# Kernel optimization log

Hardware: AMD Instinct MI355X
Metric: run time of the kernel (lower is better)

Reference implementation:

```python
import jax, jax.numpy as jnp
import numpy as np

B, T, H, V, S = 64, 32, 512, 32000, 400


def setup_inputs() -> dict:
    key = jax.random.key(0)
    ks = jax.random.split(key, 14)
    f = lambda k, s: jax.random.normal(k, s, dtype=jnp.float32)
    return {
        "inputs": jax.random.randint(ks[0], (B, T), 0, V),
        "embedding0": f(ks[1], (B, H)),
        "output0": f(ks[2], (B, H)),
        "tree_h0": f(ks[3], (B, H)),
        "tree_c0": f(ks[4], (B, H)),
        "tree_context": f(ks[5], (B, S, H)),
        "text_h0": f(ks[6], (B, H)),
        "text_c0": f(ks[7], (B, H)),
        "text_context": f(ks[8], (B, S, H)),
        "word_emb": f(ks[9], (V, H)) * 0.02,
        "Wx": f(ks[10], (2 * H, 4 * H)) * 0.02,   # LSTM input weights (input_size = 2H)
        "Wh": f(ks[11], (H, 4 * H)) * 0.02,       # LSTM recurrent weights
        "b": jnp.zeros((4 * H,), jnp.float32),
        "W_in": f(ks[12], (H, H)) * 0.02,         # attention score projection
        "W_out": f(ks[13], (4 * H, H)) * 0.02,    # attention combine projection
    }


def _lstm_cell(x, h, c, Wx, Wh, b):
    g = x @ Wx + h @ Wh + b                      # [B,4H]
    i, f, gg, o = jnp.split(g, 4, axis=-1)
    c_new = jax.nn.sigmoid(f) * c + jax.nn.sigmoid(i) * jnp.tanh(gg)
    h_new = jax.nn.sigmoid(o) * jnp.tanh(c_new)
    return h_new, c_new


def _attend(h, ctx, W_in):
    target = h @ W_in                             # [B,H]
    scores = jnp.einsum('bsh,bh->bs', ctx, target)
    attn = jax.nn.softmax(scores, axis=-1)
    return jnp.einsum('bs,bsh->bh', attn, ctx)    # weighted context [B,H]


def reference(inputs, embedding0, output0, tree_h0, tree_c0, tree_context,
              text_h0, text_c0, text_context, word_emb, Wx, Wh, b, W_in, W_out):
    embeddings = word_emb[inputs]                 # [B,T,H]
    embeddings = jnp.transpose(embeddings, (1, 0, 2))  # time-major [T,B,H]

    def step(carry, emb_i):
        emb, out, th, tc, xh, xc = carry
        x = jnp.concatenate([emb, out], axis=1)   # [B,2H]
        th, tc = _lstm_cell(x, th, tc, Wx, Wh, b)  # tree branch (shared weights)
        xh, xc = _lstm_cell(x, xh, xc, Wx, Wh, b)  # text branch (shared weights)
        w_tree = _attend(th, tree_context, W_in)
        w_text = _attend(xh, text_context, W_in)
        combined = jnp.concatenate([w_tree, w_text, th, xh], axis=1)  # [B,4H]
        out = jnp.tanh(combined @ W_out)           # dropout = identity (eval mode)
        return (emb_i, out, th, tc, xh, xc), out

    carry0 = (embedding0, output0, tree_h0, tree_c0, text_h0, text_c0)
    _, outs = jax.lax.scan(step, carry0, embeddings)  # outs: [T,B,H]
    return jnp.transpose(outs, (1, 0, 2))             # [B,T,H]
```

## Files before the change

### kernel.cpp

```cpp
#include <hip/hip_runtime.h>
#include <hip/hip_bf16.h>
#include <math.h>

#define BB 64
#define TT 32
#define HH 512
#define H2 1024
#define H4 2048
#define SS 400

#define OFF_WT_HI 0u
#define OFF_WT_LO 1572864u
#define OFF_WIT_HI 3145728u
#define OFF_WIT_LO 3276800u
#define OFF_EH    3407872u
#define OFF_EL    3932160u
#define OFF_OH    4456448u
#define OFF_OL    4472832u
#define OFF_HHP   4489216u
#define OFF_HLP   4521984u
#define OFF_TC    4554752u
#define OFF_XC    4620288u
#define OFF_TH    4685824u
#define OFF_XH    4751360u
#define OFF_G     4816896u
#define OFF_TGTP  6914048u
#define OFF_PACC  7438336u
#define OFF_PML   7962624u
#define OFF_CTX16 7964672u
#define WS_NEED_F 21071872u
#define OFF_WOT_HI 21071872u
#define OFF_WOT_LO 21596160u
#define OFF_COMBH  22120448u
#define OFF_COMBL  22153216u
#define WS_NEED2_F 22185984u
#define OFF_PART  OFF_G

typedef short bf16x8 __attribute__((ext_vector_type(8)));
typedef float f32x4  __attribute__((ext_vector_type(4)));

__device__ __forceinline__ float sigm(float x){ return 1.f/(1.f+__expf(-x)); }

__device__ __forceinline__ unsigned short bf_rn(float x){
  unsigned int u = __float_as_uint(x);
  return (unsigned short)((u + 0x7fffu + ((u>>16)&1u)) >> 16);
}
__device__ __forceinline__ void split2(float x, unsigned short &h, unsigned short &l){
  h = bf_rn(x);
  float hf = __uint_as_float(((unsigned int)h)<<16);
  l = bf_rn(x - hf);
}
__device__ __forceinline__ float blo(unsigned int u){ return __uint_as_float(u<<16); }
__device__ __forceinline__ float bhi(unsigned int u){ return __uint_as_float(u & 0xffff0000u); }

__global__ __launch_bounds__(256) void k_wprep(const float* __restrict__ Wx,
    const float* __restrict__ Wh, unsigned short* __restrict__ wt_hi,
    unsigned short* __restrict__ wt_lo){
  __shared__ float lds[64][68];
  int bk = blockIdx.x >> 5, bn = blockIdx.x & 31;
  int k0 = bk*64, n0 = bn*64;
  int tid = threadIdx.x;
  #pragma unroll
  for (int i=0;i<4;i++){
    int flat = tid + i*256;
    int k = flat >> 4, nq = flat & 15;
    int kg = k0 + k;
    const float* srow = (kg < 1024) ? Wx + (size_t)kg*H4 : Wh + (size_t)(kg-1024)*H4;
    float4 v = *(const float4*)(srow + n0 + nq*4);
    *(float4*)&lds[k][nq*4] = v;
  }
  __syncthreads();
  #pragma unroll
  for (int i=0;i<2;i++){
    int flat = tid + i*256;
    int n = flat >> 3, k8 = flat & 7;
    ushort4 h0, h1, l0, l1;
    unsigned short h[8], l[8];
    #pragma unroll
    for (int j=0;j<8;j++) split2(lds[k8*8+j][n], h[j], l[j]);
    h0.x=h[0];h0.y=h[1];h0.z=h[2];h0.w=h[3]; h1.x=h[4];h1.y=h[5];h1.z=h[6];h1.w=h[7];
    l0.x=l[0];l0.y=l[1];l0.z=l[2];l0.w=l[3]; l1.x=l[4];l1.y=l[5];l1.z=l[6];l1.w=l[7];
    size_t dst = (size_t)(n0+n)*1536 + k0 + k8*8;
    *(ushort4*)(wt_hi+dst) = h0; *(ushort4*)(wt_hi+dst+4) = h1;
    *(ushort4*)(wt_lo+dst) = l0; *(ushort4*)(wt_lo+dst+4) = l1;
  }
}

__global__ __launch_bounds__(256) void k_wiprep(const float* __restrict__ W_in,
    unsigned short* __restrict__ wit_hi, unsigned short* __restrict__ wit_lo){
  __shared__ float lds[64][68];
  int bk = blockIdx.x >> 3, bn = blockIdx.x & 7;
  int k0 = bk*64, n0 = bn*64;
  int tid = threadIdx.x;
  #pragma unroll
  for (int i=0;i<4;i++){
    int flat = tid + i*256;
    int k = flat >> 4, nq = flat & 15;
    float4 v = *(const float4*)(W_in + (size_t)(k0+k)*HH + n0 + nq*4);
    *(float4*)&lds[k][nq*4] = v;
  }
  __syncthreads();
  #pragma unroll
  for (int i=0;i<2;i++){
    int flat = tid + i*256;
    int n = flat >> 3, k8 = flat & 7;
    ushort4 h0, h1, l0, l1;
    unsigned short h[8], l[8];
    #pragma unroll
    for (int j=0;j<8;j++) split2(lds[k8*8+j][n], h[j], l[j]);
    h0.x=h[0];h0.y=h[1];h0.z=h[2];h0.w=h[3]; h1.x=h[4];h1.y=h[5];h1.z=h[6];h1.w=h[7];
    l0.x=l[0];l0.y=l[1];l0.z=l[2];l0.w=l[3]; l1.x=l[4];l1.y=l[5];l1.z=l[6];l1.w=l[7];
    size_t dst = (size_t)(n0+n)*HH + k0 + k8*8;
    *(ushort4*)(wit_hi+dst) = h0; *(ushort4*)(wit_hi+dst+4) = h1;
    *(ushort4*)(wit_lo+dst) = l0; *(ushort4*)(wit_lo+dst+4) = l1;
  }
}

__global__ __launch_bounds__(256) void k_woprep(const float* __restrict__ W_out,
    unsigned short* __restrict__ wot_hi, unsigned short* __restrict__ wot_lo){
  __shared__ float lds[64][68];
  int bk = blockIdx.x >> 3, bn = blockIdx.x & 7;
  int k0 = bk*64, n0 = bn*64;
  int tid = threadIdx.x;
  #pragma unroll
  for (int i=0;i<4;i++){
    int flat = tid + i*256;
    int k = flat >> 4, nq = flat & 15;
    float4 v = *(const float4*)(W_out + (size_t)(k0+k)*HH + n0 + nq*4);
    *(float4*)&lds[k][nq*4] = v;
  }
  __syncthreads();
  #pragma unroll
  for (int i=0;i<2;i++){
    int flat = tid + i*256;
    int n = flat >> 3, k8 = flat & 7;
    ushort4 h0, h1, l0, l1;
    unsigned short h[8], l[8];
    #pragma unroll
    for (int j=0;j<8;j++) split2(lds[k8*8+j][n], h[j], l[j]);
    h0.x=h[0];h0.y=h[1];h0.z=h[2];h0.w=h[3]; h1.x=h[4];h1.y=h[5];h1.z=h[6];h1.w=h[7];
    l0.x=l[0];l0.y=l[1];l0.z=l[2];l0.w=l[3]; l1.x=l[4];l1.y=l[5];l1.z=l[6];l1.w=l[7];
    size_t dst = (size_t)(n0+n)*H4 + k0 + k8*8;
    *(ushort4*)(wot_hi+dst) = h0; *(ushort4*)(wot_hi+dst+4) = h1;
    *(ushort4*)(wot_lo+dst) = l0; *(ushort4*)(wot_lo+dst+4) = l1;
  }
}

__global__ __launch_bounds__(256) void k_ctx16(const float* __restrict__ trctx,
    const float* __restrict__ txctx, unsigned short* __restrict__ ctx16){
  size_t gid = (size_t)blockIdx.x*256 + threadIdx.x;
  size_t off = gid*8;
  const size_t CH = (size_t)BB*SS*HH;
  const float* src = (off < CH) ? trctx + off : txctx + (off - CH);
  float4 a = *(const float4*)src;
  float4 c = *(const float4*)(src+4);
  ushort4 u0, u1;
  u0.x=bf_rn(a.x); u0.y=bf_rn(a.y); u0.z=bf_rn(a.z); u0.w=bf_rn(a.w);
  u1.x=bf_rn(c.x); u1.y=bf_rn(c.y); u1.z=bf_rn(c.z); u1.w=bf_rn(c.w);
  *(ushort4*)(ctx16+off) = u0;
  *(ushort4*)(ctx16+off+4) = u1;
}

__global__ __launch_bounds__(128) void k_prep(const int* __restrict__ inp,
    const float* __restrict__ emb0, const float* __restrict__ wemb,
    unsigned short* __restrict__ eh, unsigned short* __restrict__ el){
  int n = blockIdx.x; int t = n >> 6, b = n & 63;
  const float* src = (t==0) ? emb0 + (size_t)b*HH
                            : wemb + (size_t)inp[b*TT + (t-1)]*HH;
  float4 v = ((const float4*)src)[threadIdx.x];
  ushort4 h, l;
  split2(v.x,h.x,l.x); split2(v.y,h.y,l.y); split2(v.z,h.z,l.z); split2(v.w,h.w,l.w);
  size_t base = ((size_t)t*BB + b)*HH + threadIdx.x*4;
  *(ushort4*)(eh+base) = h; *(ushort4*)(el+base) = l;
}

__global__ __launch_bounds__(256) void k_init(const float* __restrict__ th0,
    const float* __restrict__ tc0, const float* __restrict__ xh0,
    const float* __restrict__ xc0, const float* __restrict__ out0,
    float* __restrict__ ws){
  unsigned short* hhp = (unsigned short*)(ws + OFF_HHP);
  unsigned short* hlp = (unsigned short*)(ws + OFF_HLP);
  unsigned short* oh  = (unsigned short*)(ws + OFF_OH);
  unsigned short* ol  = (unsigned short*)(ws + OFF_OL);
  int which = blockIdx.x >> 5;
  int idx = (blockIdx.x & 31)*256 + threadIdx.x;
  if (which==0){ ((float4*)(ws+OFF_TC))[idx] = ((const float4*)tc0)[idx]; return; }
  if (which==1){ ((float4*)(ws+OFF_XC))[idx] = ((const float4*)xc0)[idx]; return; }
  const float* s = which==2? th0 : which==3? xh0 : out0;
  float4 v = ((const float4*)s)[idx];
  ushort4 h, l;
  split2(v.x,h.x,l.x); split2(v.y,h.y,l.y); split2(v.z,h.z,l.z); split2(v.w,h.w,l.w);
  if (which==4){
    *(ushort4*)(oh + (size_t)idx*4) = h; *(ushort4*)(ol + (size_t)idx*4) = l;
  } else {
    size_t base = (size_t)(which-2)*BB*HH + (size_t)idx*4;
    *(ushort4*)(hhp+base) = h; *(ushort4*)(hlp+base) = l;
  }
}

__global__ __launch_bounds__(256) void k_gemm(const unsigned short* __restrict__ wt_hi,
    const unsigned short* __restrict__ wt_lo, const unsigned short* __restrict__ eh,
    const unsigned short* __restrict__ el, const unsigned short* __restrict__ oh,
    const unsigned short* __restrict__ ol, const unsigned short* __restrict__ hhp,
    const unsigned short* __restrict__ hlp, float* __restrict__ gpart, int t){
  int tid = threadIdx.x, lane = tid & 63, wave = tid >> 6;
  int bn = blockIdx.x & 31, ks = blockIdx.x >> 5;
  int lm = lane & 15, lk = (lane >> 4) << 3;
  f32x4 acc[2][4];
  #pragma unroll
  for (int i=0;i<2;i++)
    #pragma unroll
    for (int j=0;j<4;j++) acc[i][j] = (f32x4){0.f,0.f,0.f,0.f};
  size_t ebase[2], obase[2], hbase[2];
  #pragma unroll
  for (int i=0;i<2;i++){
    int r = (wave*2 + i)*16 + lm;
    int b = r & 63, br = r >> 6;
    ebase[i] = ((size_t)t*BB + b)*HH;
    obase[i] = (size_t)b*HH;
    hbase[i] = ((size_t)br*BB + b)*HH;
  }
  size_t wb[4];
  #pragma unroll
  for (int j=0;j<4;j++) wb[j] = (size_t)(bn*64 + j*16 + lm)*1536;
  #pragma unroll
  for (int c=0;c<6;c++){
    int kc = ks*192 + c*32;
    int sec = kc >> 9;
    int kk = (kc & 511) + lk;
    const unsigned short* ph = sec==0? eh : sec==1? oh : hhp;
    const unsigned short* pl = sec==0? el : sec==1? ol : hlp;
    bf16x8 ah[2], al[2], wh_[4], wl_[4];
    #pragma unroll
    for (int i=0;i<2;i++){
      size_t off = (sec==0? ebase[i] : sec==1? obase[i] : hbase[i]) + kk;
      ah[i] = *(const bf16x8*)(ph + off);
      al[i] = *(const bf16x8*)(pl + off);
    }
    int kw = kc + lk;
    #pragma unroll
    for (int j=0;j<4;j++){
      wh_[j] = *(const bf16x8*)(wt_hi + wb[j] + kw);
      wl_[j] = *(const bf16x8*)(wt_lo + wb[j] + kw);
    }
    #pragma unroll
    for (int i=0;i<2;i++)
      #pragma unroll
      for (int j=0;j<4;j++){
        acc[i][j] = __builtin_amdgcn_mfma_f32_16x16x32_bf16(ah[i], wh_[j], acc[i][j], 0,0,0);
        acc[i][j] = __builtin_amdgcn_mfma_f32_16x16x32_bf16(ah[i], wl_[j], acc[i][j], 0,0,0);
        acc[i][j] = __builtin_amdgcn_mfma_f32_16x16x32_bf16(al[i], wh_[j], acc[i][j], 0,0,0);
      }
  }
  int lr4 = (lane >> 4) * 4;
  #pragma unroll
  for (int i=0;i<2;i++){
    int m0 = (wave*2+i)*16;
    #pragma unroll
    for (int j=0;j<4;j++){
      int col = bn*64 + j*16 + lm;
      #pragma unroll
      for (int q=0;q<4;q++){
        int row = m0 + lr4 + q;
        gpart[((size_t)ks*128 + row)*H4 + col] = acc[i][j][q];
      }
    }
  }
}

__global__ __launch_bounds__(256) void k_lstm(float* __restrict__ ws,
    const float* __restrict__ bias, int rs){
  int gid = blockIdx.x*256 + threadIdx.x;
  int b = gid >> 9, j = gid & 511;
  int wsl = rs ^ 1;
  const float* gp = ws + OFF_G;
  unsigned short* hhp = (unsigned short*)(ws + OFF_HHP);
  unsigned short* hlp = (unsigned short*)(ws + OFF_HLP);
  #pragma unroll
  for (int br=0;br<2;br++){
    float g0=0.f,g1=0.f,g2=0.f,g3=0.f;
    #pragma unroll
    for (int ks=0;ks<8;ks++){
      size_t base = ((size_t)ks*128 + br*64 + b)*H4 + j;
      g0 += gp[base]; g1 += gp[base+512]; g2 += gp[base+1024]; g3 += gp[base+1536];
    }
    g0 += bias[j]; g1 += bias[512+j]; g2 += bias[1024+j]; g3 += bias[1536+j];
    size_t hoff = (br? OFF_XH : OFF_TH), coff = (br? OFF_XC : OFF_TC);
    float cold = ws[coff + (size_t)rs*BB*HH + (size_t)b*HH + j];
    float cn = sigm(g1)*cold + sigm(g0)*tanhf(g2);
    float hn = sigm(g3)*tanhf(cn);
    ws[coff + (size_t)wsl*BB*HH + (size_t)b*HH + j] = cn;
    ws[hoff + (size_t)wsl*BB*HH + (size_t)b*HH + j] = hn;
    unsigned short h_, l_;
    split2(hn, h_, l_);
    hhp[(size_t)(br*64+b)*HH + j] = h_;
    hlp[(size_t)(br*64+b)*HH + j] = l_;
  }
}

__global__ __launch_bounds__(256) void k_tgtB(const unsigned short* __restrict__ wit_hi,
    const unsigned short* __restrict__ wit_lo, const unsigned short* __restrict__ hhp,
    const unsigned short* __restrict__ hlp, float* __restrict__ tgtp){
  int tid = threadIdx.x, lane = tid & 63, wave = tid >> 6;
  int cn = blockIdx.x & 7, ks = blockIdx.x >> 3;
  int lm = lane & 15, lk = (lane >> 4) << 3;
  f32x4 acc[2][4];
  #pragma unroll
  for (int i=0;i<2;i++)
    #pragma unroll
    for (int j=0;j<4;j++) acc[i][j] = (f32x4){0.f,0.f,0.f,0.f};
  size_t abase[2];
  #pragma unroll
  for (int i=0;i<2;i++) abase[i] = (size_t)(wave*32 + i*16 + lm)*HH;
  size_t wb[4];
  #pragma unroll
  for (int j=0;j<4;j++) wb[j] = (size_t)(cn*64 + j*16 + lm)*HH;
  #pragma unroll
  for (int c=0;c<2;c++){
    int kc = ks*64 + c*32;
    bf16x8 ah[2], al[2], wh_[4], wl_[4];
    #pragma unroll
    for (int i=0;i<2;i++){
      ah[i] = *(const bf16x8*)(hhp + abase[i] + kc + lk);
      al[i] = *(const bf16x8*)(hlp + abase[i] + kc + lk);
    }
    #pragma unroll
    for (int j=0;j<4;j++){
      wh_[j] = *(const bf16x8*)(wit_hi + wb[j] + kc + lk);
      wl_[j] = *(const bf16x8*)(wit_lo + wb[j] + kc + lk);
    }
    #pragma unroll
    for (int i=0;i<2;i++)
      #pragma unroll
      for (int j=0;j<4;j++){
        acc[i][j] = __builtin_amdgcn_mfma_f32_16x16x32_bf16(ah[i], wh_[j], acc[i][j], 0,0,0);
        acc[i][j] = __builtin_amdgcn_mfma_f32_16x16x32_bf16(ah[i], wl_[j], acc[i][j], 0,0,0);
        acc[i][j] = __builtin_amdgcn_mfma_f32_16x16x32_bf16(al[i], wh_[j], acc[i][j], 0,0,0);
      }
  }
  int lr4 = (lane >> 4) * 4;
  #pragma unroll
  for (int i=0;i<2;i++){
    int m0 = wave*32 + i*16;
    #pragma unroll
    for (int j=0;j<4;j++){
      int col = cn*64 + j*16 + lm;
      #pragma unroll
      for (int q=0;q<4;q++){
        int row = m0 + lr4 + q;
        tgtp[((size_t)ks*128 + row)*HH + col] = acc[i][j][q];
      }
    }
  }
}

__global__ __launch_bounds__(512, 8) void k_attn(const float* __restrict__ tree_ctx,
    const float* __restrict__ text_ctx, const unsigned short* __restrict__ ctx16,
    float* __restrict__ ws, int use16){
  int blk = blockIdx.x;
  int sh = blk & 7, b = (blk>>3) & 63, branch = blk >> 9;
  int tid = threadIdx.x, lane = tid & 63, wave = tid >> 6;
  __shared__ float tgt_s[512];
  __shared__ float sc_s[64];
  __shared__ float w_s[64];
  __shared__ float accs[8][512];
  int row128 = branch*64 + b;
  if (tid < 128){
    float4 s = {0,0,0,0};
    #pragma unroll
    for (int p=0;p<8;p++){
      float4 v = *(const float4*)(ws + OFF_TGTP + ((size_t)p*128 + row128)*HH + tid*4);
      s.x += v.x; s.y += v.y; s.z += v.z; s.w += v.w;
    }
    ((float4*)tgt_s)[tid] = s;
  }
  if (tid >= 128 && tid < 192) sc_s[tid-128] = -INFINITY;
  __syncthreads();
  const size_t CH = (size_t)BB*SS*HH;
  const float* ctxf = (branch? text_ctx : tree_ctx) + ((size_t)b*SS + sh*50)*HH;
  const unsigned short* c16 = ctx16 + (branch? CH:0) + ((size_t)b*SS + sh*50)*HH;
  float4 ta = *(const float4*)&tgt_s[lane*8];
  float4 tb = *(const float4*)&tgt_s[lane*8+4];
  if (use16){
    for (int r = wave; r < 50; r += 8){
      uint4 u = *(const uint4*)(c16 + (size_t)r*HH + lane*8);
      float p = blo(u.x)*ta.x + bhi(u.x)*ta.y + blo(u.y)*ta.z + bhi(u.y)*ta.w
              + blo(u.z)*tb.x + bhi(u.z)*tb.y + blo(u.w)*tb.z + bhi(u.w)*tb.w;
      #pragma unroll
      for (int off=32; off; off>>=1) p += __shfl_xor(p, off, 64);
      if (lane==0) sc_s[r] = p;
    }
  } else {
    for (int r = wave; r < 50; r += 8){
      const float* crow = ctxf + (size_t)r*HH + lane*8;
      float4 ca = *(const float4*)crow;
      float4 cb = *(const float4*)(crow+4);
      float p = ca.x*ta.x + ca.y*ta.y + ca.z*ta.z + ca.w*ta.w
              + cb.x*tb.x + cb.y*tb.y + cb.z*tb.z + cb.w*tb.w;
      #pragma unroll
      for (int off=32; off; off>>=1) p += __shfl_xor(p, off, 64);
      if (lane==0) sc_s[r] = p;
    }
  }
  __syncthreads();
  if (wave==0){
    float s = sc_s[lane];
    float m = s;
    #pragma unroll
    for (int off=32; off; off>>=1) m = fmaxf(m, __shfl_xor(m, off, 64));
    float e = (lane<50)? __expf(s-m) : 0.f;
    w_s[lane] = e;
    float l = e;
    #pragma unroll
    for (int off=32; off; off>>=1) l += __shfl_xor(l, off, 64);
    if (lane==0){
      int pidx = (branch*64 + b)*8 + sh;
      ws[OFF_PML + (size_t)pidx*2]   = m;
      ws[OFF_PML + (size_t)pidx*2+1] = l;
    }
  }
  __syncthreads();
  float a[8] = {0,0,0,0,0,0,0,0};
  if (use16){
    for (int r = wave; r < 50; r += 8){
      float w = w_s[r];
      uint4 u = *(const uint4*)(c16 + (size_t)r*HH + lane*8);
      a[0] += w*blo(u.x); a[1] += w*bhi(u.x);
      a[2] += w*blo(u.y); a[3] += w*bhi(u.y);
      a[4] += w*blo(u.z); a[5] += w*bhi(u.z);
      a[6] += w*blo(u.w); a[7] += w*bhi(u.w);
    }
  } else {
    for (int r = wave; r < 50; r += 8){
      float w = w_s[r];
      const float* crow = ctxf + (size_t)r*HH + lane*8;
      float4 ca = *(const float4*)crow;
      float4 cb = *(const float4*)(crow+4);
      a[0] += w*ca.x; a[1] += w*ca.y; a[2] += w*ca.z; a[3] += w*ca.w;
      a[4] += w*cb.x; a[5] += w*cb.y; a[6] += w*cb.z; a[7] += w*cb.w;
    }
  }
  #pragma unroll
  for (int j=0;j<8;j++) accs[wave][lane*8+j] = a[j];
  __syncthreads();
  float s = 0.f;
  #pragma unroll
  for (int w8=0;w8<8;w8++) s += accs[w8][tid];
  int pidx = (branch*64 + b)*8 + sh;
  ws[OFF_PACC + (size_t)pidx*HH + tid] = s;
}

__global__ __launch_bounds__(256) void k_outA(float* __restrict__ ws){
  __shared__ float ce_s[2][8];
  int b = blockIdx.x, tid = threadIdx.x;
  if (tid < 2){
    int p0 = (tid*64 + b)*8;
    float mv[8], lv[8];
    float M = -INFINITY;
    #pragma unroll
    for (int i=0;i<8;i++){
      mv[i] = ws[OFF_PML + (size_t)(p0+i)*2];
      lv[i] = ws[OFF_PML + (size_t)(p0+i)*2+1];
      M = fmaxf(M, mv[i]);
    }
    float L = 0.f, ev[8];
    #pragma unroll
    for (int i=0;i<8;i++){ ev[i] = __expf(mv[i]-M); L += lv[i]*ev[i]; }
    #pragma unroll
    for (int i=0;i<8;i++) ce_s[tid][i] = ev[i]/L;
  }
  __syncthreads();
  int h = tid*4;
  int sec = h >> 9, hs = h & 511;
  int p0 = (sec*64 + b)*8;
  float4 v = {0,0,0,0};
  #pragma unroll
  for (int p=0;p<8;p++){
    float4 a = *(const float4*)(ws + OFF_PACC + (size_t)(p0+p)*HH + hs);
    float cw = ce_s[sec][p];
    v.x += a.x*cw; v.y += a.y*cw; v.z += a.z*cw; v.w += a.w*cw;
  }
  ushort4 hv, lv;
  split2(v.x,hv.x,lv.x); split2(v.y,hv.y,lv.y); split2(v.z,hv.z,lv.z); split2(v.w,hv.w,lv.w);
  unsigned short* ch = (unsigned short*)(ws + OFF_COMBH);
  unsigned short* cl = (unsigned short*)(ws + OFF_COMBL);
  *(ushort4*)(ch + (size_t)b*1024 + h) = hv;
  *(ushort4*)(cl + (size_t)b*1024 + h) = lv;
}

__global__ __launch_bounds__(256) void k_outBF(const unsigned short* __restrict__ wot_hi,
    const unsigned short* __restrict__ wot_lo, const unsigned short* __restrict__ combh,
    const unsigned short* __restrict__ combl, const unsigned short* __restrict__ hhp,
    const unsigned short* __restrict__ hlp, float* __restrict__ dout,
    unsigned short* __restrict__ oh, unsigned short* __restrict__ ol, int t){
  __shared__ float accs[4][16][17];
  int tid = threadIdx.x, lane = tid & 63, wave = tid >> 6;
  int nt = blockIdx.x & 31, mt = blockIdx.x >> 5;
  int lm = lane & 15, lk = (lane >> 4) << 3;
  f32x4 acc = (f32x4){0.f,0.f,0.f,0.f};
  int b = mt*16 + lm;
  int col = nt*16 + lm;
  size_t wb = (size_t)col*H4 + (size_t)wave*512;
  const unsigned short *pa_h, *pa_l;
  size_t abase;
  if (wave < 2){ pa_h = combh; pa_l = combl; abase = (size_t)b*1024 + (size_t)wave*512; }
  else         { pa_h = hhp;   pa_l = hlp;   abase = ((size_t)(wave-2)*64 + b)*HH; }
  #pragma unroll
  for (int c=0;c<16;c++){
    int kk = c*32 + lk;
    bf16x8 ah  = *(const bf16x8*)(pa_h + abase + kk);
    bf16x8 al  = *(const bf16x8*)(pa_l + abase + kk);
    bf16x8 wh_ = *(const bf16x8*)(wot_hi + wb + kk);
    bf16x8 wl_ = *(const bf16x8*)(wot_lo + wb + kk);
    acc = __builtin_amdgcn_mfma_f32_16x16x32_bf16(ah, wh_, acc, 0,0,0);
    acc = __builtin_amdgcn_mfma_f32_16x16x32_bf16(ah, wl_, acc, 0,0,0);
    acc = __builtin_amdgcn_mfma_f32_16x16x32_bf16(al, wh_, acc, 0,0,0);
  }
  int lr4 = (lane >> 4) * 4;
  #pragma unroll
  for (int q=0;q<4;q++) accs[wave][lr4+q][lm] = acc[q];
  __syncthreads();
  int row = tid >> 4, colL = tid & 15;
  float s = accs[0][row][colL] + accs[1][row][colL]
          + accs[2][row][colL] + accs[3][row][colL];
  float v = tanhf(s);
  int bb = mt*16 + row, cc = nt*16 + colL;
  dout[((size_t)bb*TT + t)*HH + cc] = v;
  unsigned short h_, l_;
  split2(v, h_, l_);
  oh[(size_t)bb*HH + cc] = h_;
  ol[(size_t)bb*HH + cc] = l_;
}

__global__ __launch_bounds__(256) void k_outB(const float* __restrict__ W_out,
    float* __restrict__ ws, int wsl){
  __shared__ float comb_s[16][256];
  __shared__ float ce_s[16][8];
  int tid = threadIdx.x, lane = tid & 63, wave = tid >> 6;
  int blk = blockIdx.x;
  int ct = blk & 7, bg = (blk>>3)&3, ks = blk>>5;
  int b0 = bg*16;
  int k0 = ks*256;
  int sec = ks >> 1;
  int kk0 = (ks & 1)*256;
  int c = ct*64 + lane;
  if (sec < 2){
    if (tid < 16){
      int b = b0 + tid;
      int p0 = (sec*64 + b)*8;
      float mv[8], lv[8];
      float M = -INFINITY;
      #pragma unroll
      for (int i=0;i<8;i++){
        mv[i] = ws[OFF_PML + (size_t)(p0+i)*2];
        lv[i] = ws[OFF_PML + (size_t)(p0+i)*2+1];
        M = fmaxf(M, mv[i]);
      }
      float L = 0.f, ev[8];
      #pragma unroll
      for (int i=0;i<8;i++){ ev[i] = __expf(mv[i]-M); L += lv[i]*ev[i]; }
      #pragma unroll
      for (int i=0;i<8;i++) ce_s[tid][i] = ev[i]/L;
    }
    __syncthreads();
  }
  #pragma unroll
  for (int i=0;i<4;i++){
    int flat = tid + i*256;
    int row = flat >> 6;
    int q   = flat & 63;
    int b = b0 + row;
    int h = kk0 + q*4;
    float4 v;
    if (sec < 2){
      int p0 = (sec*64 + b)*8;
      v.x = 0.f; v.y = 0.f; v.z = 0.f; v.w = 0.f;
      #pragma unroll
      for (int p=0;p<8;p++){
        float4 a = *(const float4*)(ws + OFF_PACC + (size_t)(p0+p)*HH + h);
        float cw = ce_s[row][p];
        v.x += a.x*cw; v.y += a.y*cw; v.z += a.z*cw; v.w += a.w*cw;
      }
    } else {
      size_t hoff = (sec==2 ? OFF_TH : OFF_XH) + (size_t)wsl*BB*HH;
      v = *(const float4*)(ws + hoff + (size_t)b*HH + h);
    }
    *(float4*)&comb_s[row][q*4] = v;
  }
  __syncthreads();
  float acc[4] = {0,0,0,0};
  #pragma unroll 4
  for (int k=0;k<256;k++){
    float wv = W_out[(size_t)(k0+k)*HH + c];
    #pragma unroll
    for (int i=0;i<4;i++) acc[i] += comb_s[wave*4+i][k]*wv;
  }
  #pragma unroll
  for (int i=0;i<4;i++){
    int b = b0 + wave*4 + i;
    ws[OFF_PART + ((size_t)ks*BB + b)*HH + c] = acc[i];
  }
}

__global__ __launch_bounds__(256) void k_outC(float* __restrict__ ws,
    float* __restrict__ dout, int t){
  int gid = blockIdx.x*256 + threadIdx.x;
  int b = gid >> 7, cq = gid & 127;
  int c0 = cq*4;
  float4 s = {0,0,0,0};
  #pragma unroll
  for (int ks=0;ks<8;ks++){
    float4 p = *(const float4*)(ws + OFF_PART + ((size_t)ks*BB + b)*HH + c0);
    s.x += p.x; s.y += p.y; s.z += p.z; s.w += p.w;
  }
  float4 o;
  o.x = tanhf(s.x); o.y = tanhf(s.y); o.z = tanhf(s.z); o.w = tanhf(s.w);
  *(float4*)(dout + ((size_t)b*TT + t)*HH + c0) = o;
  ushort4 h, l;
  split2(o.x,h.x,l.x); split2(o.y,h.y,l.y); split2(o.z,h.z,l.z); split2(o.w,h.w,l.w);
  unsigned short* oh = (unsigned short*)(ws + OFF_OH);
  unsigned short* ol = (unsigned short*)(ws + OFF_OL);
  *(ushort4*)(oh + (size_t)b*HH + c0) = h;
  *(ushort4*)(ol + (size_t)b*HH + c0) = l;
}

extern "C" void kernel_launch(void* const* d_in, const int* in_sizes, int n_in,
                              void* d_out, int out_size, void* d_ws, size_t ws_size,
                              hipStream_t stream){
  const int*   inp   = (const int*)  d_in[0];
  const float* emb0  = (const float*)d_in[1];
  const float* out0  = (const float*)d_in[2];
  const float* th0   = (const float*)d_in[3];
  const float* tc0   = (const float*)d_in[4];
  const float* trctx = (const float*)d_in[5];
  const float* xh0   = (const float*)d_in[6];
  const float* xc0   = (const float*)d_in[7];
  const float* txctx = (const float*)d_in[8];
  const float* wemb  = (const float*)d_in[9];
  const float* Wx    = (const float*)d_in[10];
  const float* Wh    = (const float*)d_in[11];
  const float* bias  = (const float*)d_in[12];
  const float* W_in  = (const float*)d_in[13];
  const float* W_out = (const float*)d_in[14];
  float* ws  = (float*)d_ws;
  float* out = (float*)d_out;
  unsigned short* wt_hi  = (unsigned short*)(ws + OFF_WT_HI);
  unsigned short* wt_lo  = (unsigned short*)(ws + OFF_WT_LO);
  unsigned short* wit_hi = (unsigned short*)(ws + OFF_WIT_HI);
  unsigned short* wit_lo = (unsigned short*)(ws + OFF_WIT_LO);
  unsigned short* wot_hi = (unsigned short*)(ws + OFF_WOT_HI);
  unsigned short* wot_lo = (unsigned short*)(ws + OFF_WOT_LO);
  unsigned short* combh  = (unsigned short*)(ws + OFF_COMBH);
  unsigned short* combl  = (unsigned short*)(ws + OFF_COMBL);
  unsigned short* eh  = (unsigned short*)(ws + OFF_EH);
  unsigned short* el  = (unsigned short*)(ws + OFF_EL);
  unsigned short* oh  = (unsigned short*)(ws + OFF_OH);
  unsigned short* ol  = (unsigned short*)(ws + OFF_OL);
  unsigned short* hhp = (unsigned short*)(ws + OFF_HHP);
  unsigned short* hlp = (unsigned short*)(ws + OFF_HLP);
  unsigned short* ctx16 = (unsigned short*)(ws + OFF_CTX16);
  float* gpart = ws + OFF_G;
  float* tgtp  = ws + OFF_TGTP;
  int use16 = (ws_size >= (size_t)WS_NEED_F  * 4u) ? 1 : 0;
  int fast  = (ws_size >= (size_t)WS_NEED2_F * 4u) ? 1 : 0;

  hipLaunchKernelGGL(k_wprep,  dim3(768),   dim3(256), 0, stream, Wx, Wh, wt_hi, wt_lo);
  hipLaunchKernelGGL(k_wiprep, dim3(64),    dim3(256), 0, stream, W_in, wit_hi, wit_lo);
  if (fast)
    hipLaunchKernelGGL(k_woprep, dim3(256), dim3(256), 0, stream, W_out, wot_hi, wot_lo);
  if (use16)
    hipLaunchKernelGGL(k_ctx16, dim3(12800), dim3(256), 0, stream, trctx, txctx, ctx16);
  hipLaunchKernelGGL(k_prep,   dim3(TT*BB), dim3(128), 0, stream, inp, emb0, wemb, eh, el);
  hipLaunchKernelGGL(k_init,   dim3(160),   dim3(256), 0, stream, th0, tc0, xh0, xc0, out0, ws);
  for (int t=0; t<TT; t++){
    int rs = t & 1, wsl = rs ^ 1;
    hipLaunchKernelGGL(k_gemm, dim3(256),  dim3(256), 0, stream,
                       wt_hi, wt_lo, eh, el, oh, ol, hhp, hlp, gpart, t);
    hipLaunchKernelGGL(k_lstm, dim3(128),  dim3(256), 0, stream, ws, bias, rs);
    hipLaunchKernelGGL(k_tgtB, dim3(64),   dim3(256), 0, stream, wit_hi, wit_lo, hhp, hlp, tgtp);
    hipLaunchKernelGGL(k_attn, dim3(1024), dim3(512), 0, stream, trctx, txctx, ctx16, ws, use16);
    if (fast){
      hipLaunchKernelGGL(k_outA,  dim3(64),  dim3(256), 0, stream, ws);
      hipLaunchKernelGGL(k_outBF, dim3(128), dim3(256), 0, stream,
                         wot_hi, wot_lo, combh, combl, hhp, hlp, out, oh, ol, t);
    } else {
      hipLaunchKernelGGL(k_outB, dim3(256), dim3(256), 0, stream, W_out, ws, wsl);
      hipLaunchKernelGGL(k_outC, dim3(32),  dim3(256), 0, stream, ws, out, t);
    }
  }
}
```

Before: 1.653 ms.

## Replace split-K target projection with full-K tiles and drop partial-sum reduction

The target projection kernel now gives each block a 16-row M tile and a 64-column slice and runs the full K loop of 512 in each wave. This removes the 8-way split-K partial buffers, and the attention kernel now reads a single target row instead of summing eight partials. The context bf16 conversion is also split into two launches, one per context tensor, which removes a per-thread branch. The cost is a longer serial MFMA dependency chain per wave and more total loads of the hidden state and weights in the target kernel.

```diff
diff --git a/kernel.cpp b/kernel.cpp
--- a/kernel.cpp
+++ b/kernel.cpp
@@ -146,19 +146,16 @@
   }
 }
 
-__global__ __launch_bounds__(256) void k_ctx16(const float* __restrict__ trctx,
-    const float* __restrict__ txctx, unsigned short* __restrict__ ctx16){
-  size_t gid = (size_t)blockIdx.x*256 + threadIdx.x;
-  size_t off = gid*8;
-  const size_t CH = (size_t)BB*SS*HH;
-  const float* src = (off < CH) ? trctx + off : txctx + (off - CH);
-  float4 a = *(const float4*)src;
-  float4 c = *(const float4*)(src+4);
+__global__ __launch_bounds__(256) void k_ctx16(const float* __restrict__ src,
+    unsigned short* __restrict__ dst){
+  size_t off = ((size_t)blockIdx.x*256 + threadIdx.x)*8;
+  float4 a = *(const float4*)(src + off);
+  float4 c = *(const float4*)(src + off + 4);
   ushort4 u0, u1;
   u0.x=bf_rn(a.x); u0.y=bf_rn(a.y); u0.z=bf_rn(a.z); u0.w=bf_rn(a.w);
   u1.x=bf_rn(c.x); u1.y=bf_rn(c.y); u1.z=bf_rn(c.z); u1.w=bf_rn(c.w);
-  *(ushort4*)(ctx16+off) = u0;
-  *(ushort4*)(ctx16+off+4) = u1;
+  *(ushort4*)(dst+off) = u0;
+  *(ushort4*)(dst+off+4) = u1;
 }
 
 __global__ __launch_bounds__(128) void k_prep(const int* __restrict__ inp,
@@ -300,58 +297,29 @@
 
 __global__ __launch_bounds__(256) void k_tgtB(const unsigned short* __restrict__ wit_hi,
     const unsigned short* __restrict__ wit_lo, const unsigned short* __restrict__ hhp,
-    const unsigned short* __restrict__ hlp, float* __restrict__ tgtp){
+    const unsigned short* __restrict__ hlp, float* __restrict__ tgt){
   int tid = threadIdx.x, lane = tid & 63, wave = tid >> 6;
-  int cn = blockIdx.x & 7, ks = blockIdx.x >> 3;
+  int cn = blockIdx.x & 7, mt = blockIdx.x >> 3;
   int lm = lane & 15, lk = (lane >> 4) << 3;
-  f32x4 acc[2][4];
-  #pragma unroll
-  for (int i=0;i<2;i++)
-    #pragma unroll
-    for (int j=0;j<4;j++) acc[i][j] = (f32x4){0.f,0.f,0.f,0.f};
-  size_t abase[2];
-  #pragma unroll
-  for (int i=0;i<2;i++) abase[i] = (size_t)(wave*32 + i*16 + lm)*HH;
-  size_t wb[4];
-  #pragma unroll
-  for (int j=0;j<4;j++) wb[j] = (size_t)(cn*64 + j*16 + lm)*HH;
-  #pragma unroll
-  for (int c=0;c<2;c++){
-    int kc = ks*64 + c*32;
-    bf16x8 ah[2], al[2], wh_[4], wl_[4];
-    #pragma unroll
-    for (int i=0;i<2;i++){
-      ah[i] = *(const bf16x8*)(hhp + abase[i] + kc + lk);
-      al[i] = *(const bf16x8*)(hlp + abase[i] + kc + lk);
-    }
-    #pragma unroll
-    for (int j=0;j<4;j++){
-      wh_[j] = *(const bf16x8*)(wit_hi + wb[j] + kc + lk);
-      wl_[j] = *(const bf16x8*)(wit_lo + wb[j] + kc + lk);
-    }
-    #pragma unroll
-    for (int i=0;i<2;i++)
-      #pragma unroll
-      for (int j=0;j<4;j++){
-        acc[i][j] = __builtin_amdgcn_mfma_f32_16x16x32_bf16(ah[i], wh_[j], acc[i][j], 0,0,0);
-        acc[i][j] = __builtin_amdgcn_mfma_f32_16x16x32_bf16(ah[i], wl_[j], acc[i][j], 0,0,0);
-        acc[i][j] = __builtin_amdgcn_mfma_f32_16x16x32_bf16(al[i], wh_[j], acc[i][j], 0,0,0);
-      }
+  f32x4 acc = (f32x4){0.f,0.f,0.f,0.f};
+  size_t abase = (size_t)(mt*16 + lm)*HH;
+  size_t wb = (size_t)(cn*64 + wave*16 + lm)*HH;
+  #pragma unroll
+  for (int c=0;c<16;c++){
+    int kc = c*32 + lk;
+    bf16x8 ah  = *(const bf16x8*)(hhp + abase + kc);
+    bf16x8 al  = *(const bf16x8*)(hlp + abase + kc);
+    bf16x8 wh_ = *(const bf16x8*)(wit_hi + wb + kc);
+    bf16x8 wl_ = *(const bf16x8*)(wit_lo + wb + kc);
+    acc = __builtin_amdgcn_mfma_f32_16x16x32_bf16(ah, wh_, acc, 0,0,0);
+    acc = __builtin_amdgcn_mfma_f32_16x16x32_bf16(ah, wl_, acc, 0,0,0);
+    acc = __builtin_amdgcn_mfma_f32_16x16x32_bf16(al, wh_, acc, 0,0,0);
   }
   int lr4 = (lane >> 4) * 4;
-  #pragma unroll
-  for (int i=0;i<2;i++){
-    int m0 = wave*32 + i*16;
-    #pragma unroll
-    for (int j=0;j<4;j++){
-      int col = cn*64 + j*16 + lm;
-      #pragma unroll
-      for (int q=0;q<4;q++){
-        int row = m0 + lr4 + q;
-        tgtp[((size_t)ks*128 + row)*HH + col] = acc[i][j][q];
-      }
-    }
-  }
+  int col = cn*64 + wave*16 + lm;
+  #pragma unroll
+  for (int q=0;q<4;q++)
+    tgt[(size_t)(mt*16 + lr4 + q)*HH + col] = acc[q];
 }
 
 __global__ __launch_bounds__(512, 8) void k_attn(const float* __restrict__ tree_ctx,
@@ -365,15 +333,8 @@
   __shared__ float w_s[64];
   __shared__ float accs[8][512];
   int row128 = branch*64 + b;
-  if (tid < 128){
-    float4 s = {0,0,0,0};
-    #pragma unroll
-    for (int p=0;p<8;p++){
-      float4 v = *(const float4*)(ws + OFF_TGTP + ((size_t)p*128 + row128)*HH + tid*4);
-      s.x += v.x; s.y += v.y; s.z += v.z; s.w += v.w;
-    }
-    ((float4*)tgt_s)[tid] = s;
-  }
+  if (tid < 128)
+    ((float4*)tgt_s)[tid] = ((const float4*)(ws + OFF_TGTP + (size_t)row128*HH))[tid];
   if (tid >= 128 && tid < 192) sc_s[tid-128] = -INFINITY;
   __syncthreads();
   const size_t CH = (size_t)BB*SS*HH;
@@ -660,16 +621,19 @@
   unsigned short* hlp = (unsigned short*)(ws + OFF_HLP);
   unsigned short* ctx16 = (unsigned short*)(ws + OFF_CTX16);
   float* gpart = ws + OFF_G;
-  float* tgtp  = ws + OFF_TGTP;
+  float* tgt   = ws + OFF_TGTP;
   int use16 = (ws_size >= (size_t)WS_NEED_F  * 4u) ? 1 : 0;
   int fast  = (ws_size >= (size_t)WS_NEED2_F * 4u) ? 1 : 0;
+  const size_t CH = (size_t)BB*SS*HH;
 
   hipLaunchKernelGGL(k_wprep,  dim3(768),   dim3(256), 0, stream, Wx, Wh, wt_hi, wt_lo);
   hipLaunchKernelGGL(k_wiprep, dim3(64),    dim3(256), 0, stream, W_in, wit_hi, wit_lo);
   if (fast)
     hipLaunchKernelGGL(k_woprep, dim3(256), dim3(256), 0, stream, W_out, wot_hi, wot_lo);
-  if (use16)
-    hipLaunchKernelGGL(k_ctx16, dim3(12800), dim3(256), 0, stream, trctx, txctx, ctx16);
+  if (use16){
+    hipLaunchKernelGGL(k_ctx16, dim3(6400), dim3(256), 0, stream, trctx, ctx16);
+    hipLaunchKernelGGL(k_ctx16, dim3(6400), dim3(256), 0, stream, txctx, ctx16 + CH);
+  }
   hipLaunchKernelGGL(k_prep,   dim3(TT*BB), dim3(128), 0, stream, inp, emb0, wemb, eh, el);
   hipLaunchKernelGGL(k_init,   dim3(160),   dim3(256), 0, stream, th0, tc0, xh0, xc0, out0, ws);
   for (int t=0; t<TT; t++){
@@ -677,7 +641,7 @@
     hipLaunchKernelGGL(k_gemm, dim3(256),  dim3(256), 0, stream,
                        wt_hi, wt_lo, eh, el, oh, ol, hhp, hlp, gpart, t);
     hipLaunchKernelGGL(k_lstm, dim3(128),  dim3(256), 0, stream, ws, bias, rs);
-    hipLaunchKernelGGL(k_tgtB, dim3(64),   dim3(256), 0, stream, wit_hi, wit_lo, hhp, hlp, tgtp);
+    hipLaunchKernelGGL(k_tgtB, dim3(64),   dim3(256), 0, stream, wit_hi, wit_lo, hhp, hlp, tgt);
     hipLaunchKernelGGL(k_attn, dim3(1024), dim3(512), 0, stream, trctx, txctx, ctx16, ws, use16);
     if (fast){
       hipLaunchKernelGGL(k_outA,  dim3(64),  dim3(256), 0, stream, ws);
```

Measured after the change: 1.718 ms. 1.04x slower.
